# Performance work log

Measured on AMD Instinct MI355X. Metric: run time of the kernel, lower is better.

## Reference

```python
import jax, jax.numpy as jnp
import numpy as np

B, N, D = 8, 1024, 768
H = 12
HD = D // H


def setup_inputs() -> dict:
    key = jax.random.key(0)
    ks = jax.random.split(key, 9)
    s = 1.0 / np.sqrt(D)
    return {
        "x": jax.random.normal(ks[0], (B, N, D), dtype=jnp.float32),
        "Wq": jax.random.normal(ks[1], (D, D), dtype=jnp.float32) * s,
        "bq": jax.random.normal(ks[2], (D,), dtype=jnp.float32) * 0.02,
        "Wk": jax.random.normal(ks[3], (D, D), dtype=jnp.float32) * s,
        "bk": jax.random.normal(ks[4], (D,), dtype=jnp.float32) * 0.02,
        "Wv": jax.random.normal(ks[5], (D, D), dtype=jnp.float32) * s,
        "bv": jax.random.normal(ks[6], (D,), dtype=jnp.float32) * 0.02,
        "Wo": jax.random.normal(ks[7], (D, D), dtype=jnp.float32) * s,
        "bo": jax.random.normal(ks[8], (D,), dtype=jnp.float32) * 0.02,
    }


def _softmax_one(x):
    # quiet softmax: exp(x - max) / (1 + sum exp(x - max))
    x = x - jnp.max(x, axis=-1, keepdims=True)
    ex = jnp.exp(x)
    return ex / (1.0 + jnp.sum(ex, axis=-1, keepdims=True))


def reference(x, Wq, bq, Wk, bk, Wv, bv, Wo, bo):
    q = x @ Wq + bq  # [B,N,D]
    k = x @ Wk + bk
    v = x @ Wv + bv
    # split heads -> [B,H,N,HD]
    qs = q.reshape(B, N, H, HD).transpose(0, 2, 1, 3)
    ks = k.reshape(B, N, H, HD).transpose(0, 2, 1, 3)
    vs = v.reshape(B, N, H, HD).transpose(0, 2, 1, 3)
    scores = jnp.einsum("bhqd,bhkd->bhqk", qs, ks) / np.sqrt(HD)
    attn = _softmax_one(scores)  # quiet_attention=True
    ctx = jnp.einsum("bhqk,bhkd->bhqd", attn, vs)
    ctx = ctx.transpose(0, 2, 1, 3).reshape(B, N, D)
    return ctx @ Wo + bo
```

## Files before the change

kernel.cpp:

```cpp
#include <hip/hip_runtime.h>
#include <cstdint>

#define DEV __device__ __forceinline__

typedef __bf16 bf16x4 __attribute__((ext_vector_type(4)));
typedef __bf16 bf16x8 __attribute__((ext_vector_type(8)));
typedef float  floatx2 __attribute__((ext_vector_type(2)));
typedef float  floatx4 __attribute__((ext_vector_type(4)));
typedef float  floatx16 __attribute__((ext_vector_type(16)));
typedef unsigned uint4v __attribute__((ext_vector_type(4)));

constexpr int BB = 8, NSEQ = 1024, DMODEL = 768, NH = 12, HD = 64;
constexpr int MTOK = BB * NSEQ;
constexpr int NQKV = 3 * DMODEL;
constexpr float CS = 0.18033688011112042f;

DEV void async_copy16(void* lds, const void* g) {
    __builtin_amdgcn_global_load_lds(
        (__attribute__((address_space(1))) void*)(const_cast<void*>(g)),
        (__attribute__((address_space(3))) void*)lds,
        16, 0, 0);
}

DEV floatx4 mfma16x32(bf16x8 a, bf16x8 b, floatx4 c) {
    return __builtin_amdgcn_mfma_f32_16x16x32_bf16(a, b, c, 0, 0, 0);
}
DEV floatx16 mfma32x16(bf16x8 a, bf16x8 b, floatx16 c) {
    return __builtin_amdgcn_mfma_f32_32x32x16_bf16(a, b, c, 0, 0, 0);
}
DEV unsigned cvtpk(float a, float b) {
    unsigned r;
    asm("v_cvt_pk_bf16_f32 %0, %1, %2" : "=v"(r) : "v"(a), "v"(b));
    return r;
}
DEV void swap32(unsigned& x, unsigned& y) {
    asm("v_permlane32_swap_b32 %0, %1" : "+v"(x), "+v"(y));
}


__global__ __launch_bounds__(256) void k_prep(const float* __restrict__ x,
                                              __bf16* __restrict__ xb,
                                              const float* __restrict__ Wq,
                                              const float* __restrict__ Wk,
                                              const float* __restrict__ Wv,
                                              const float* __restrict__ Wo,
                                              __bf16* __restrict__ wtqkv,
                                              __bf16* __restrict__ wto,
                                              const float* __restrict__ bq,
                                              const float* __restrict__ bk,
                                              const float* __restrict__ bv,
                                              float* __restrict__ bqkv) {
    __shared__ float tile[32][33];
    int bid = blockIdx.x, t = threadIdx.x;
    if (bid < 6144) {
        int i = (bid * 256 + t) * 4;
        float4 v = *(const float4*)(x + i);
        bf16x4 o;
        o[0] = (__bf16)v.x; o[1] = (__bf16)v.y; o[2] = (__bf16)v.z; o[3] = (__bf16)v.w;
        *(bf16x4*)(xb + i) = o;
    } else if (bid < 8448) {
        int idx = bid - 6144;
        int z = idx / 576, rem = idx % 576;
        int k0 = (rem % 24) * 32, n0 = (rem / 24) * 32;
        const float* W = (z == 0) ? Wq : (z == 1) ? Wk : (z == 2) ? Wv : Wo;
        int tx = t & 31, ty = t >> 5;
#pragma unroll
        for (int p = 0; p < 4; p++)
            tile[ty + 8 * p][tx] = W[(size_t)(k0 + ty + 8 * p) * 768 + n0 + tx];
        __syncthreads();
        __bf16* out = (z < 3) ? (wtqkv + (size_t)z * 768 * 768) : wto;
#pragma unroll
        for (int p = 0; p < 4; p++)
            out[(size_t)(n0 + ty + 8 * p) * 768 + k0 + tx] = (__bf16)tile[tx][ty + 8 * p];
    } else {
        int i = (bid - 8448) * 256 + t;
        if (i < 768) bqkv[i] = bq[i];
        else if (i < 1536) bqkv[i] = bk[i - 768];
        else bqkv[i] = bv[i - 1536];
    }
}

__global__ __launch_bounds__(256) void k_qkv(const __bf16* __restrict__ A,
                                             const __bf16* __restrict__ Bt,
                                             const float* __restrict__ bias,
                                             __bf16* __restrict__ qfb,
                                             __bf16* __restrict__ kfb,
                                             __bf16* __restrict__ vfb) {
    constexpr int SLOT = 16384;
    __shared__ __align__(16) __bf16 lds[2 * SLOT];
    int t = threadIdx.x, lane = t & 63, w = t >> 6;
    int quad = lane >> 4, n16 = lane & 15;
    int wm = w & 1, wn = w >> 1;
    int m0 = blockIdx.x * 128, n0 = blockIdx.y * 128;
    floatx4 acc[4][4] = {};

    auto stage_tile = [&](__bf16* slot, int k0) {
        __bf16* As_ = slot;
        __bf16* Bs_ = slot + 8192;
#pragma unroll
        for (int i = 0; i < 4; i++) {
            int off = t + i * 256;
            int row = off >> 3, pc = off & 7;
            int c = pc ^ (row & 7);
            async_copy16(&As_[row * 64 + pc * 8],
                         &A[(size_t)(m0 + row) * 768 + k0 + c * 8]);
        }
#pragma unroll
        for (int i = 0; i < 4; i++) {
            int off = t + i * 256;
            int row = off >> 3, pc = off & 7;
            int c = pc ^ (row & 7);
            async_copy16(&Bs_[row * 64 + pc * 8],
                         &Bt[(size_t)(n0 + row) * 768 + k0 + c * 8]);
        }
    };

    stage_tile(lds, 0);

#pragma unroll
    for (int kt = 0; kt < 12; kt++) {
        __bf16* As_ = lds + (kt & 1) * SLOT;
        __bf16* Bs_ = As_ + 8192;

        if (kt + 1 < 12) stage_tile(lds + ((kt + 1) & 1) * SLOT, (kt + 1) * 64);
        __builtin_amdgcn_sched_barrier(0);
        if (kt + 1 < 12) {
            asm volatile("s_waitcnt vmcnt(8)\n\ts_barrier" ::: "memory");
        } else {
            asm volatile("s_waitcnt vmcnt(0)\n\ts_barrier" ::: "memory");
        }
        __builtin_amdgcn_sched_barrier(0);

#pragma unroll
        for (int kfi = 0; kfi < 2; kfi++) {
            bf16x8 a[4], bfr[4];
#pragma unroll
            for (int rt = 0; rt < 4; rt++) {
                int row = wm * 64 + rt * 16 + n16;
                a[rt] = *(const bf16x8*)&As_[row * 64 + ((quad + 4 * kfi) ^ (row & 7)) * 8];
            }
#pragma unroll
            for (int ct = 0; ct < 4; ct++) {
                int row = wn * 64 + ct * 16 + n16;
                bfr[ct] = *(const bf16x8*)&Bs_[row * 64 + ((quad + 4 * kfi) ^ (row & 7)) * 8];
            }
            __builtin_amdgcn_s_setprio(1);
#pragma unroll
            for (int rt = 0; rt < 4; rt++)
#pragma unroll
                for (int ct = 0; ct < 4; ct++)
                    acc[rt][ct] = mfma16x32(a[rt], bfr[ct], acc[rt][ct]);
            __builtin_amdgcn_s_setprio(0);
        }

        if (kt + 1 < 12) {
            __builtin_amdgcn_sched_barrier(0);
            asm volatile("s_barrier" ::: "memory");
            __builtin_amdgcn_sched_barrier(0);
        }
    }

    if (n0 >= 1536) {
#pragma unroll
        for (int ct = 0; ct < 4; ct++) {
            int col = n0 + wn * 64 + ct * 16 + n16;
            float bs = bias[col];
            int cz = col - 1536;
            int hh = cz >> 6, hd = cz & 63;
            int mg = hd >> 5, l5v = hd & 31;
#pragma unroll
            for (int rt = 0; rt < 4; rt++) {
                int row0 = m0 + wm * 64 + rt * 16 + quad * 4;
                int bb = row0 >> 10, key = row0 & 1023;
                int iw = key >> 7, w_ = (key >> 5) & 3, kc = (key >> 4) & 1;
                int b5v = (key >> 3) & 1, j0 = key & 7;
                bf16x4 pk;
#pragma unroll
                for (int r = 0; r < 4; r++) pk[r] = (__bf16)(acc[rt][ct][r] + bs);
                size_t idx = (((((size_t)(bb * 12 + hh) * 8 + iw) * 4 + w_) * 2 + kc) * 2 + mg) * 512
                             + (size_t)(b5v * 32 + l5v) * 8 + j0;
                *(bf16x4*)&vfb[idx] = pk;
            }
        }
    } else {
        __bf16* dst = (n0 < 768) ? qfb : kfb;
        float mult = (n0 < 768) ? CS : 1.0f;
        bool isQ = (n0 < 768);
        int cofs = isQ ? 0 : 768;
#pragma unroll
        for (int ct = 0; ct < 4; ct++) {
            int col = n0 + wn * 64 + ct * 16 + n16;
            float bs = bias[col];
            int cz = col - cofs;
            int hh = cz >> 6, hd = cz & 63;
            int kfi = hd >> 4, b5v = (hd >> 3) & 1, j = hd & 7;
#pragma unroll
            for (int rt = 0; rt < 4; rt++) {
                int row0 = m0 + wm * 64 + rt * 16 + quad * 4;
                int bb = row0 >> 10, q10 = row0 & 1023;
                size_t idx;
                if (isQ) {
                    int qt = q10 >> 5, l5v = q10 & 31;
                    idx = (((size_t)(bb * 12 + hh) * 32 + qt) * 4 + kfi) * 512
                          + (size_t)(b5v * 32 + l5v) * 8 + j;
                } else {
                    int iw = q10 >> 7, w_ = (q10 >> 5) & 3, l5v = q10 & 31;
                    idx = ((((size_t)(bb * 12 + hh) * 8 + iw) * 4 + w_) * 4 + kfi) * 512
                          + (size_t)(b5v * 32 + l5v) * 8 + j;
                }
#pragma unroll
                for (int r = 0; r < 4; r++)
                    dst[idx + (size_t)r * 8] = (__bf16)((acc[rt][ct][r] + bs) * mult);
            }
        }
    }
}

__global__ __launch_bounds__(256) void k_oproj(const __bf16* __restrict__ A,
                                               const __bf16* __restrict__ Bt,
                                               const float* __restrict__ bias,
                                               float* __restrict__ C) {
    constexpr int SLOT = 12288;
    __shared__ __align__(16) __bf16 lds[2 * SLOT];
    int t = threadIdx.x, lane = t & 63, w = t >> 6;
    int quad = lane >> 4, n16 = lane & 15;
    int wm = w & 1, wn = w >> 1;
    int m0 = blockIdx.x * 128, n0 = blockIdx.y * 64;
    floatx4 acc[4][2] = {};

    auto stage_tile = [&](__bf16* slot, int k0) {
        __bf16* As_ = slot;
        __bf16* Bs_ = slot + 8192;
#pragma unroll
        for (int i = 0; i < 4; i++) {
            int off = t + i * 256;
            int row = off >> 3, pc = off & 7;
            int c = pc ^ (row & 7);
            async_copy16(&As_[row * 64 + pc * 8],
                         &A[(size_t)(m0 + row) * 768 + k0 + c * 8]);
        }
#pragma unroll
        for (int i = 0; i < 2; i++) {
            int off = t + i * 256;
            int row = off >> 3, pc = off & 7;
            int c = pc ^ (row & 7);
            async_copy16(&Bs_[row * 64 + pc * 8],
                         &Bt[(size_t)(n0 + row) * 768 + k0 + c * 8]);
        }
    };

    stage_tile(lds, 0);

#pragma unroll
    for (int kt = 0; kt < 12; kt++) {
        __bf16* As_ = lds + (kt & 1) * SLOT;
        __bf16* Bs_ = As_ + 8192;

        if (kt + 1 < 12) stage_tile(lds + ((kt + 1) & 1) * SLOT, (kt + 1) * 64);
        __builtin_amdgcn_sched_barrier(0);
        if (kt + 1 < 12) {
            asm volatile("s_waitcnt vmcnt(6)\n\ts_barrier" ::: "memory");
        } else {
            asm volatile("s_waitcnt vmcnt(0)\n\ts_barrier" ::: "memory");
        }
        __builtin_amdgcn_sched_barrier(0);

#pragma unroll
        for (int kfi = 0; kfi < 2; kfi++) {
            bf16x8 a[4], bfr[2];
#pragma unroll
            for (int rt = 0; rt < 4; rt++) {
                int row = wm * 64 + rt * 16 + n16;
                a[rt] = *(const bf16x8*)&As_[row * 64 + ((quad + 4 * kfi) ^ (row & 7)) * 8];
            }
#pragma unroll
            for (int ct = 0; ct < 2; ct++) {
                int row = wn * 32 + ct * 16 + n16;
                bfr[ct] = *(const bf16x8*)&Bs_[row * 64 + ((quad + 4 * kfi) ^ (row & 7)) * 8];
            }
            __builtin_amdgcn_s_setprio(1);
#pragma unroll
            for (int rt = 0; rt < 4; rt++)
#pragma unroll
                for (int ct = 0; ct < 2; ct++)
                    acc[rt][ct] = mfma16x32(a[rt], bfr[ct], acc[rt][ct]);
            __builtin_amdgcn_s_setprio(0);
        }

        if (kt + 1 < 12) {
            __builtin_amdgcn_sched_barrier(0);
            asm volatile("s_barrier" ::: "memory");
            __builtin_amdgcn_sched_barrier(0);
        }
    }

#pragma unroll
    for (int ct = 0; ct < 2; ct++) {
        int col = n0 + wn * 32 + ct * 16 + n16;
        float bs = bias[col];
#pragma unroll
        for (int rt = 0; rt < 4; rt++) {
#pragma unroll
            for (int r = 0; r < 4; r++) {
                int row = m0 + wm * 64 + rt * 16 + quad * 4 + r;
                C[(size_t)row * DMODEL + col] = acc[rt][ct][r] + bs;
            }
        }
    }
}

__global__ __launch_bounds__(256) void k_attn(const __bf16* __restrict__ QF,
                                              const __bf16* __restrict__ KF,
                                              const __bf16* __restrict__ VF,
                                              __bf16* __restrict__ ctx) {
    int t = threadIdx.x, lane = t & 63, w = t >> 6;
    int l5 = lane & 31, b5 = lane >> 5;
    int id = blockIdx.x;
    int bB = id & 7;
    int seq = id >> 3;
    int h = seq % 12;
    int qb = seq / 12;
    int qt = qb * 4 + w;
    int bh = bB * NH + h;

    bf16x8 qf[4];
    {
        const __bf16* qp = QF + ((size_t)(bh * 32 + qt) * 4) * 512 + lane * 8;
#pragma unroll
        for (int kfi = 0; kfi < 4; kfi++)
            qf[kfi] = *(const bf16x8*)(qp + kfi * 512);
    }
    const __bf16* kp = KF + (size_t)(bh * 32) * 2048 + lane * 8;
    const __bf16* vp = VF + (size_t)(bh * 32) * 2048 + lane * 8;

    floatx16 acc[2] = {};
    floatx2 rs2 = {0.f, 0.f};
    float pm = 0.f;

    auto compute = [&](bf16x8 (&kf)[4], bf16x8 (&vf)[4]) {
        floatx16 s = {};
#pragma unroll
        for (int kfi = 0; kfi < 4; kfi++)
            s = mfma32x16(kf[kfi], qf[kfi], s);
        float p[16];
#pragma unroll
        for (int r = 0; r < 16; r++)
            p[r] = __builtin_amdgcn_exp2f(s[r]);
#pragma unroll
        for (int r = 0; r < 16; r += 2) {
            floatx2 pp = {p[r], p[r + 1]};
            rs2 += pp;
            pm = fmaxf(fmaxf(p[r], p[r + 1]), pm);
        }
        unsigned x0 = cvtpk(p[0], p[1]),   y0 = cvtpk(p[4], p[5]);
        unsigned x1 = cvtpk(p[2], p[3]),   y1 = cvtpk(p[6], p[7]);
        unsigned x2 = cvtpk(p[8], p[9]),   y2 = cvtpk(p[12], p[13]);
        unsigned x3 = cvtpk(p[10], p[11]), y3 = cvtpk(p[14], p[15]);
        swap32(x0, y0); swap32(x1, y1); swap32(x2, y2); swap32(x3, y3);
        uint4v pa = {x0, x1, y0, y1};
        uint4v pbv = {x2, x3, y2, y3};
        bf16x8 P0 = __builtin_bit_cast(bf16x8, pa);
        bf16x8 P1 = __builtin_bit_cast(bf16x8, pbv);
        acc[0] = mfma32x16(vf[0], P0, acc[0]);
        acc[1] = mfma32x16(vf[1], P0, acc[1]);
        acc[0] = mfma32x16(vf[2], P1, acc[0]);
        acc[1] = mfma32x16(vf[3], P1, acc[1]);
    };

    bf16x8 ka[4], kb[4], va[4], vb[4];
#pragma unroll
    for (int f = 0; f < 4; f++) ka[f] = *(const bf16x8*)(kp + f * 512);
#pragma unroll
    for (int f = 0; f < 4; f++) va[f] = *(const bf16x8*)(vp + f * 512);
    kp += 2048; vp += 2048;

    for (int c = 0; c < 32; c += 2) {
#pragma unroll
        for (int f = 0; f < 4; f++) kb[f] = *(const bf16x8*)(kp + f * 512);
#pragma unroll
        for (int f = 0; f < 4; f++) vb[f] = *(const bf16x8*)(vp + f * 512);
        kp += 2048; vp += 2048;
        compute(ka, va);
        if (c < 30) {
#pragma unroll
            for (int f = 0; f < 4; f++) ka[f] = *(const bf16x8*)(kp + f * 512);
#pragma unroll
            for (int f = 0; f < 4; f++) va[f] = *(const bf16x8*)(vp + f * 512);
            kp += 2048; vp += 2048;
        }
        compute(kb, vb);
    }

    float rs = rs2[0] + rs2[1];
    rs += __shfl_xor(rs, 32);
    pm = fmaxf(pm, __shfl_xor(pm, 32));
    float invd = 1.f / (pm + rs);

    __bf16* dst = ctx + ((size_t)(bB * NSEQ) + qt * 32 + l5) * DMODEL + h * 64;
#pragma unroll
    for (int mg = 0; mg < 2; mg++)
#pragma unroll
        for (int rq = 0; rq < 4; rq++) {
            bf16x4 o;
#pragma unroll
            for (int e = 0; e < 4; e++)
                o[e] = (__bf16)(acc[mg][rq * 4 + e] * invd);
            *(bf16x4*)(dst + mg * 32 + rq * 8 + b5 * 4) = o;
        }
}

extern "C" void kernel_launch(void* const* d_in, const int* in_sizes, int n_in,
                              void* d_out, int out_size, void* d_ws, size_t ws_size,
                              hipStream_t stream) {
    (void)in_sizes; (void)n_in; (void)out_size;
    const float* x  = (const float*)d_in[0];
    const float* Wq = (const float*)d_in[1];
    const float* bq = (const float*)d_in[2];
    const float* Wk = (const float*)d_in[3];
    const float* bk = (const float*)d_in[4];
    const float* Wv = (const float*)d_in[5];
    const float* bv = (const float*)d_in[6];
    const float* Wo = (const float*)d_in[7];
    const float* bo = (const float*)d_in[8];
    float* out = (float*)d_out;

    char* ws = (char*)d_ws;
    size_t off = 0;
    auto alloc = [&](size_t bytes) {
        void* p = ws + off;
        off += (bytes + 255) & ~(size_t)255;
        return p;
    };
    __bf16* xb    = (__bf16*)alloc((size_t)MTOK * DMODEL * 2);
    __bf16* wtqkv = (__bf16*)alloc((size_t)NQKV * DMODEL * 2);
    __bf16* wto   = (__bf16*)alloc((size_t)DMODEL * DMODEL * 2);
    float*  bqkv  = (float*)alloc((size_t)NQKV * 4);
    __bf16* qfb   = (__bf16*)alloc((size_t)MTOK * DMODEL * 2);
    __bf16* kfb   = (__bf16*)alloc((size_t)MTOK * DMODEL * 2);
    __bf16* vfb   = (__bf16*)alloc((size_t)MTOK * DMODEL * 2);
    if (off > ws_size) return;
    __bf16* ctx = xb;

    k_prep<<<dim3(8457), dim3(256), 0, stream>>>(x, xb, Wq, Wk, Wv, Wo, wtqkv, wto,
                                                 bq, bk, bv, bqkv);
    k_qkv<<<dim3(64, 18), dim3(256), 0, stream>>>(xb, wtqkv, bqkv, qfb, kfb, vfb);
    k_attn<<<dim3(768), dim3(256), 0, stream>>>(qfb, kfb, vfb, ctx);
    k_oproj<<<dim3(64, 12), dim3(256), 0, stream>>>(ctx, wto, bo, out);
}
```

Measured before the change: 177.5 us.

## Stage K/V tiles into LDS with async double-buffered global_load_lds in attention

```diff
diff --git a/kernel.cpp b/kernel.cpp
--- a/kernel.cpp
+++ b/kernel.cpp
@@ -313,6 +313,8 @@
                                               const __bf16* __restrict__ KF,
                                               const __bf16* __restrict__ VF,
                                               __bf16* __restrict__ ctx) {
+    constexpr int SLOT = 8192;
+    __shared__ __align__(16) __bf16 lds[2 * SLOT];
     int t = threadIdx.x, lane = t & 63, w = t >> 6;
     int l5 = lane & 31, b5 = lane >> 5;
     int id = blockIdx.x;
@@ -330,14 +332,36 @@
         for (int kfi = 0; kfi < 4; kfi++)
             qf[kfi] = *(const bf16x8*)(qp + kfi * 512);
     }
-    const __bf16* kp = KF + (size_t)(bh * 32) * 2048 + lane * 8;
-    const __bf16* vp = VF + (size_t)(bh * 32) * 2048 + lane * 8;
+    const __bf16* kbase = KF + (size_t)(bh * 32) * 2048;
+    const __bf16* vbase = VF + (size_t)(bh * 32) * 2048;
 
     floatx16 acc[2] = {};
     floatx2 rs2 = {0.f, 0.f};
     float pm = 0.f;
 
-    auto compute = [&](bf16x8 (&kf)[4], bf16x8 (&vf)[4]) {
+    auto stage = [&](int slot, int s) {
+        __bf16* ks = lds + slot * SLOT;
+        __bf16* vs = ks + 4096;
+#pragma unroll
+        for (int i = 0; i < 2; i++) {
+            int off = (t + i * 256) * 8;
+            async_copy16(&ks[off], &kbase[(size_t)s * 4096 + off]);
+        }
+#pragma unroll
+        for (int i = 0; i < 2; i++) {
+            int off = (t + i * 256) * 8;
+            async_copy16(&vs[off], &vbase[(size_t)s * 4096 + off]);
+        }
+    };
+
+    auto compute = [&](int slot, int cc) {
+        const __bf16* ks = lds + slot * SLOT + cc * 2048;
+        const __bf16* vs = lds + slot * SLOT + 4096 + cc * 2048;
+        bf16x8 kf[4], vf[4];
+#pragma unroll
+        for (int f = 0; f < 4; f++) kf[f] = *(const bf16x8*)&ks[f * 512 + lane * 8];
+#pragma unroll
+        for (int f = 0; f < 4; f++) vf[f] = *(const bf16x8*)&vs[f * 512 + lane * 8];
         floatx16 s = {};
 #pragma unroll
         for (int kfi = 0; kfi < 4; kfi++)
@@ -367,28 +391,25 @@
         acc[1] = mfma32x16(vf[3], P1, acc[1]);
     };
 
-    bf16x8 ka[4], kb[4], va[4], vb[4];
-#pragma unroll
-    for (int f = 0; f < 4; f++) ka[f] = *(const bf16x8*)(kp + f * 512);
-#pragma unroll
-    for (int f = 0; f < 4; f++) va[f] = *(const bf16x8*)(vp + f * 512);
-    kp += 2048; vp += 2048;
-
-    for (int c = 0; c < 32; c += 2) {
-#pragma unroll
-        for (int f = 0; f < 4; f++) kb[f] = *(const bf16x8*)(kp + f * 512);
-#pragma unroll
-        for (int f = 0; f < 4; f++) vb[f] = *(const bf16x8*)(vp + f * 512);
-        kp += 2048; vp += 2048;
-        compute(ka, va);
-        if (c < 30) {
-#pragma unroll
-            for (int f = 0; f < 4; f++) ka[f] = *(const bf16x8*)(kp + f * 512);
-#pragma unroll
-            for (int f = 0; f < 4; f++) va[f] = *(const bf16x8*)(vp + f * 512);
-            kp += 2048; vp += 2048;
-        }
-        compute(kb, vb);
+    stage(0, 0);
+
+    for (int s = 0; s < 16; s++) {
+        int cur = s & 1;
+        if (s + 1 < 16) stage(cur ^ 1, s + 1);
+        __builtin_amdgcn_sched_barrier(0);
+        if (s + 1 < 16) {
+            asm volatile("s_waitcnt vmcnt(4)\n\ts_barrier" ::: "memory");
+        } else {
+            asm volatile("s_waitcnt vmcnt(0)\n\ts_barrier" ::: "memory");
+        }
+        __builtin_amdgcn_sched_barrier(0);
+        compute(cur, 0);
+        compute(cur, 1);
+        if (s + 1 < 16) {
+            __builtin_amdgcn_sched_barrier(0);
+            asm volatile("s_barrier" ::: "memory");
+            __builtin_amdgcn_sched_barrier(0);
+        }
     }
 
     float rs = rs2[0] + rs2[1];
```

Result: slower. 182.0 us (+2.5%).

## Process two query tiles per wave in attention to reuse K/V fragments

Applied to the files above, without the earlier changes.

```diff
diff --git a/kernel.cpp b/kernel.cpp
--- a/kernel.cpp
+++ b/kernel.cpp
@@ -309,10 +309,10 @@
     }
 }
 
-__global__ __launch_bounds__(256) void k_attn(const __bf16* __restrict__ QF,
-                                              const __bf16* __restrict__ KF,
-                                              const __bf16* __restrict__ VF,
-                                              __bf16* __restrict__ ctx) {
+__global__ __launch_bounds__(128, 2) void k_attn(const __bf16* __restrict__ QF,
+                                                 const __bf16* __restrict__ KF,
+                                                 const __bf16* __restrict__ VF,
+                                                 __bf16* __restrict__ ctx) {
     int t = threadIdx.x, lane = t & 63, w = t >> 6;
     int l5 = lane & 31, b5 = lane >> 5;
     int id = blockIdx.x;
@@ -320,51 +320,84 @@
     int seq = id >> 3;
     int h = seq % 12;
     int qb = seq / 12;
-    int qt = qb * 4 + w;
+    int qt0 = qb * 4 + w * 2;
     int bh = bB * NH + h;
 
-    bf16x8 qf[4];
+    bf16x8 qf0[4], qf1[4];
     {
-        const __bf16* qp = QF + ((size_t)(bh * 32 + qt) * 4) * 512 + lane * 8;
-#pragma unroll
-        for (int kfi = 0; kfi < 4; kfi++)
-            qf[kfi] = *(const bf16x8*)(qp + kfi * 512);
+        const __bf16* qp = QF + ((size_t)(bh * 32 + qt0) * 4) * 512 + lane * 8;
+#pragma unroll
+        for (int kfi = 0; kfi < 4; kfi++) {
+            qf0[kfi] = *(const bf16x8*)(qp + kfi * 512);
+            qf1[kfi] = *(const bf16x8*)(qp + (4 + kfi) * 512);
+        }
     }
     const __bf16* kp = KF + (size_t)(bh * 32) * 2048 + lane * 8;
     const __bf16* vp = VF + (size_t)(bh * 32) * 2048 + lane * 8;
 
-    floatx16 acc[2] = {};
-    floatx2 rs2 = {0.f, 0.f};
-    float pm = 0.f;
+    floatx16 acc0[2] = {}, acc1[2] = {};
+    floatx2 rsa = {0.f, 0.f}, rsb = {0.f, 0.f};
+    float pma = 0.f, pmb = 0.f;
 
     auto compute = [&](bf16x8 (&kf)[4], bf16x8 (&vf)[4]) {
-        floatx16 s = {};
+        floatx16 s0 = {}, s1 = {};
 #pragma unroll
         for (int kfi = 0; kfi < 4; kfi++)
-            s = mfma32x16(kf[kfi], qf[kfi], s);
-        float p[16];
-#pragma unroll
-        for (int r = 0; r < 16; r++)
-            p[r] = __builtin_amdgcn_exp2f(s[r]);
-#pragma unroll
-        for (int r = 0; r < 16; r += 2) {
-            floatx2 pp = {p[r], p[r + 1]};
-            rs2 += pp;
-            pm = fmaxf(fmaxf(p[r], p[r + 1]), pm);
-        }
-        unsigned x0 = cvtpk(p[0], p[1]),   y0 = cvtpk(p[4], p[5]);
-        unsigned x1 = cvtpk(p[2], p[3]),   y1 = cvtpk(p[6], p[7]);
-        unsigned x2 = cvtpk(p[8], p[9]),   y2 = cvtpk(p[12], p[13]);
-        unsigned x3 = cvtpk(p[10], p[11]), y3 = cvtpk(p[14], p[15]);
-        swap32(x0, y0); swap32(x1, y1); swap32(x2, y2); swap32(x3, y3);
-        uint4v pa = {x0, x1, y0, y1};
-        uint4v pbv = {x2, x3, y2, y3};
-        bf16x8 P0 = __builtin_bit_cast(bf16x8, pa);
-        bf16x8 P1 = __builtin_bit_cast(bf16x8, pbv);
-        acc[0] = mfma32x16(vf[0], P0, acc[0]);
-        acc[1] = mfma32x16(vf[1], P0, acc[1]);
-        acc[0] = mfma32x16(vf[2], P1, acc[0]);
-        acc[1] = mfma32x16(vf[3], P1, acc[1]);
+            s0 = mfma32x16(kf[kfi], qf0[kfi], s0);
+#pragma unroll
+        for (int kfi = 0; kfi < 4; kfi++)
+            s1 = mfma32x16(kf[kfi], qf1[kfi], s1);
+
+        {
+            float p[16];
+#pragma unroll
+            for (int r = 0; r < 16; r++)
+                p[r] = __builtin_amdgcn_exp2f(s0[r]);
+#pragma unroll
+            for (int r = 0; r < 16; r += 2) {
+                floatx2 pp = {p[r], p[r + 1]};
+                rsa += pp;
+                pma = fmaxf(fmaxf(p[r], p[r + 1]), pma);
+            }
+            unsigned x0 = cvtpk(p[0], p[1]),   y0 = cvtpk(p[4], p[5]);
+            unsigned x1 = cvtpk(p[2], p[3]),   y1 = cvtpk(p[6], p[7]);
+            unsigned x2 = cvtpk(p[8], p[9]),   y2 = cvtpk(p[12], p[13]);
+            unsigned x3 = cvtpk(p[10], p[11]), y3 = cvtpk(p[14], p[15]);
+            swap32(x0, y0); swap32(x1, y1); swap32(x2, y2); swap32(x3, y3);
+            uint4v pa = {x0, x1, y0, y1};
+            uint4v pbv = {x2, x3, y2, y3};
+            bf16x8 P0 = __builtin_bit_cast(bf16x8, pa);
+            bf16x8 P1 = __builtin_bit_cast(bf16x8, pbv);
+            acc0[0] = mfma32x16(vf[0], P0, acc0[0]);
+            acc0[1] = mfma32x16(vf[1], P0, acc0[1]);
+            acc0[0] = mfma32x16(vf[2], P1, acc0[0]);
+            acc0[1] = mfma32x16(vf[3], P1, acc0[1]);
+        }
+        {
+            float p[16];
+#pragma unroll
+            for (int r = 0; r < 16; r++)
+                p[r] = __builtin_amdgcn_exp2f(s1[r]);
+#pragma unroll
+            for (int r = 0; r < 16; r += 2) {
+                floatx2 pp = {p[r], p[r + 1]};
+                rsb += pp;
+                pmb = fmaxf(fmaxf(p[r], p[r + 1]), pmb);
+            }
+            unsigned x0 = cvtpk(p[0], p[1]),   y0 = cvtpk(p[4], p[5]);
+            unsigned x1 = cvtpk(p[2], p[3]),   y1 = cvtpk(p[6], p[7]);
+            unsigned x2 = cvtpk(p[8], p[9]),   y2 = cvtpk(p[12], p[13]);
+            unsigned x3 = cvtpk(p[10], p[11]), y3 = cvtpk(p[14], p[15]);
+            swap32(x0, y0); swap32(x1, y1); swap32(x2, y2); swap32(x3, y3);
+            uint4v pa = {x0, x1, y0, y1};
+            uint4v pbv = {x2, x3, y2, y3};
+            bf16x8 P0 = __builtin_bit_cast(bf16x8, pa);
+            bf16x8 P1 = __builtin_bit_cast(bf16x8, pbv);
+            acc1[0] = mfma32x16(vf[0], P0, acc1[0]);
+            acc1[1] = mfma32x16(vf[1], P0, acc1[1]);
+            acc1[0] = mfma32x16(vf[2], P1, acc1[0]);
+            acc1[1] = mfma32x16(vf[3], P1, acc1[1]);
+        }
     };
 
     bf16x8 ka[4], kb[4], va[4], vb[4];
@@ -391,21 +424,29 @@
         compute(kb, vb);
     }
 
-    float rs = rs2[0] + rs2[1];
-    rs += __shfl_xor(rs, 32);
-    pm = fmaxf(pm, __shfl_xor(pm, 32));
-    float invd = 1.f / (pm + rs);
-
-    __bf16* dst = ctx + ((size_t)(bB * NSEQ) + qt * 32 + l5) * DMODEL + h * 64;
+    float rs0 = rsa[0] + rsa[1];
+    rs0 += __shfl_xor(rs0, 32);
+    pma = fmaxf(pma, __shfl_xor(pma, 32));
+    float invd0 = 1.f / (pma + rs0);
+    float rs1 = rsb[0] + rsb[1];
+    rs1 += __shfl_xor(rs1, 32);
+    pmb = fmaxf(pmb, __shfl_xor(pmb, 32));
+    float invd1 = 1.f / (pmb + rs1);
+
+    __bf16* dst0 = ctx + ((size_t)(bB * NSEQ) + qt0 * 32 + l5) * DMODEL + h * 64;
+    __bf16* dst1 = dst0 + (size_t)32 * DMODEL;
 #pragma unroll
     for (int mg = 0; mg < 2; mg++)
 #pragma unroll
         for (int rq = 0; rq < 4; rq++) {
-            bf16x4 o;
-#pragma unroll
-            for (int e = 0; e < 4; e++)
-                o[e] = (__bf16)(acc[mg][rq * 4 + e] * invd);
-            *(bf16x4*)(dst + mg * 32 + rq * 8 + b5 * 4) = o;
+            bf16x4 o0, o1;
+#pragma unroll
+            for (int e = 0; e < 4; e++) {
+                o0[e] = (__bf16)(acc0[mg][rq * 4 + e] * invd0);
+                o1[e] = (__bf16)(acc1[mg][rq * 4 + e] * invd1);
+            }
+            *(bf16x4*)(dst0 + mg * 32 + rq * 8 + b5 * 4) = o0;
+            *(bf16x4*)(dst1 + mg * 32 + rq * 8 + b5 * 4) = o1;
         }
 }
 
@@ -444,6 +485,6 @@
     k_prep<<<dim3(8457), dim3(256), 0, stream>>>(x, xb, Wq, Wk, Wv, Wo, wtqkv, wto,
                                                  bq, bk, bv, bqkv);
     k_qkv<<<dim3(64, 18), dim3(256), 0, stream>>>(xb, wtqkv, bqkv, qfb, kfb, vfb);
-    k_attn<<<dim3(768), dim3(256), 0, stream>>>(qfb, kfb, vfb, ctx);
+    k_attn<<<dim3(768), dim3(128), 0, stream>>>(qfb, kfb, vfb, ctx);
     k_oproj<<<dim3(64, 12), dim3(256), 0, stream>>>(ctx, wto, bo, out);
 }
```

Result: slower. 183.0 us (+3.1%).

## Shrink QKV GEMM N-tile to 64 and software-pipeline QK with softmax-PV in attention

Applied to the files above, without the earlier changes.

```diff
diff --git a/kernel.cpp b/kernel.cpp
--- a/kernel.cpp
+++ b/kernel.cpp
@@ -86,13 +86,13 @@
                                              __bf16* __restrict__ qfb,
                                              __bf16* __restrict__ kfb,
                                              __bf16* __restrict__ vfb) {
-    constexpr int SLOT = 16384;
+    constexpr int SLOT = 12288;
     __shared__ __align__(16) __bf16 lds[2 * SLOT];
     int t = threadIdx.x, lane = t & 63, w = t >> 6;
     int quad = lane >> 4, n16 = lane & 15;
     int wm = w & 1, wn = w >> 1;
-    int m0 = blockIdx.x * 128, n0 = blockIdx.y * 128;
-    floatx4 acc[4][4] = {};
+    int m0 = blockIdx.x * 128, n0 = blockIdx.y * 64;
+    floatx4 acc[4][2] = {};
 
     auto stage_tile = [&](__bf16* slot, int k0) {
         __bf16* As_ = slot;
@@ -106,7 +106,7 @@
                          &A[(size_t)(m0 + row) * 768 + k0 + c * 8]);
         }
 #pragma unroll
-        for (int i = 0; i < 4; i++) {
+        for (int i = 0; i < 2; i++) {
             int off = t + i * 256;
             int row = off >> 3, pc = off & 7;
             int c = pc ^ (row & 7);
@@ -125,7 +125,7 @@
         if (kt + 1 < 12) stage_tile(lds + ((kt + 1) & 1) * SLOT, (kt + 1) * 64);
         __builtin_amdgcn_sched_barrier(0);
         if (kt + 1 < 12) {
-            asm volatile("s_waitcnt vmcnt(8)\n\ts_barrier" ::: "memory");
+            asm volatile("s_waitcnt vmcnt(6)\n\ts_barrier" ::: "memory");
         } else {
             asm volatile("s_waitcnt vmcnt(0)\n\ts_barrier" ::: "memory");
         }
@@ -133,22 +133,22 @@
 
 #pragma unroll
         for (int kfi = 0; kfi < 2; kfi++) {
-            bf16x8 a[4], bfr[4];
+            bf16x8 a[4], bfr[2];
 #pragma unroll
             for (int rt = 0; rt < 4; rt++) {
                 int row = wm * 64 + rt * 16 + n16;
                 a[rt] = *(const bf16x8*)&As_[row * 64 + ((quad + 4 * kfi) ^ (row & 7)) * 8];
             }
 #pragma unroll
-            for (int ct = 0; ct < 4; ct++) {
-                int row = wn * 64 + ct * 16 + n16;
+            for (int ct = 0; ct < 2; ct++) {
+                int row = wn * 32 + ct * 16 + n16;
                 bfr[ct] = *(const bf16x8*)&Bs_[row * 64 + ((quad + 4 * kfi) ^ (row & 7)) * 8];
             }
             __builtin_amdgcn_s_setprio(1);
 #pragma unroll
             for (int rt = 0; rt < 4; rt++)
 #pragma unroll
-                for (int ct = 0; ct < 4; ct++)
+                for (int ct = 0; ct < 2; ct++)
                     acc[rt][ct] = mfma16x32(a[rt], bfr[ct], acc[rt][ct]);
             __builtin_amdgcn_s_setprio(0);
         }
@@ -162,8 +162,8 @@
 
     if (n0 >= 1536) {
 #pragma unroll
-        for (int ct = 0; ct < 4; ct++) {
-            int col = n0 + wn * 64 + ct * 16 + n16;
+        for (int ct = 0; ct < 2; ct++) {
+            int col = n0 + wn * 32 + ct * 16 + n16;
             float bs = bias[col];
             int cz = col - 1536;
             int hh = cz >> 6, hd = cz & 63;
@@ -188,8 +188,8 @@
         bool isQ = (n0 < 768);
         int cofs = isQ ? 0 : 768;
 #pragma unroll
-        for (int ct = 0; ct < 4; ct++) {
-            int col = n0 + wn * 64 + ct * 16 + n16;
+        for (int ct = 0; ct < 2; ct++) {
+            int col = n0 + wn * 32 + ct * 16 + n16;
             float bs = bias[col];
             int cz = col - cofs;
             int hh = cz >> 6, hd = cz & 63;
@@ -337,11 +337,14 @@
     floatx2 rs2 = {0.f, 0.f};
     float pm = 0.f;
 
-    auto compute = [&](bf16x8 (&kf)[4], bf16x8 (&vf)[4]) {
+    auto qk = [&](bf16x8 (&kf)[4]) {
         floatx16 s = {};
 #pragma unroll
         for (int kfi = 0; kfi < 4; kfi++)
             s = mfma32x16(kf[kfi], qf[kfi], s);
+        return s;
+    };
+    auto fin = [&](floatx16 s, bf16x8 (&vf)[4]) {
         float p[16];
 #pragma unroll
         for (int r = 0; r < 16; r++)
@@ -367,28 +370,38 @@
         acc[1] = mfma32x16(vf[3], P1, acc[1]);
     };
 
-    bf16x8 ka[4], kb[4], va[4], vb[4];
-#pragma unroll
-    for (int f = 0; f < 4; f++) ka[f] = *(const bf16x8*)(kp + f * 512);
-#pragma unroll
-    for (int f = 0; f < 4; f++) va[f] = *(const bf16x8*)(vp + f * 512);
+    bf16x8 k0[4], v0[4], k1[4], v1[4];
+#pragma unroll
+    for (int f = 0; f < 4; f++) k0[f] = *(const bf16x8*)(kp + f * 512);
+#pragma unroll
+    for (int f = 0; f < 4; f++) v0[f] = *(const bf16x8*)(vp + f * 512);
     kp += 2048; vp += 2048;
-
-    for (int c = 0; c < 32; c += 2) {
-#pragma unroll
-        for (int f = 0; f < 4; f++) kb[f] = *(const bf16x8*)(kp + f * 512);
-#pragma unroll
-        for (int f = 0; f < 4; f++) vb[f] = *(const bf16x8*)(vp + f * 512);
+    floatx16 s0 = qk(k0);
+
+    for (int c = 1; c < 31; c += 2) {
+#pragma unroll
+        for (int f = 0; f < 4; f++) k1[f] = *(const bf16x8*)(kp + f * 512);
+#pragma unroll
+        for (int f = 0; f < 4; f++) v1[f] = *(const bf16x8*)(vp + f * 512);
         kp += 2048; vp += 2048;
-        compute(ka, va);
-        if (c < 30) {
-#pragma unroll
-            for (int f = 0; f < 4; f++) ka[f] = *(const bf16x8*)(kp + f * 512);
-#pragma unroll
-            for (int f = 0; f < 4; f++) va[f] = *(const bf16x8*)(vp + f * 512);
-            kp += 2048; vp += 2048;
-        }
-        compute(kb, vb);
+        floatx16 s1 = qk(k1);
+        fin(s0, v0);
+#pragma unroll
+        for (int f = 0; f < 4; f++) k0[f] = *(const bf16x8*)(kp + f * 512);
+#pragma unroll
+        for (int f = 0; f < 4; f++) v0[f] = *(const bf16x8*)(vp + f * 512);
+        kp += 2048; vp += 2048;
+        s0 = qk(k0);
+        fin(s1, v1);
+    }
+    {
+#pragma unroll
+        for (int f = 0; f < 4; f++) k1[f] = *(const bf16x8*)(kp + f * 512);
+#pragma unroll
+        for (int f = 0; f < 4; f++) v1[f] = *(const bf16x8*)(vp + f * 512);
+        floatx16 s1 = qk(k1);
+        fin(s0, v0);
+        fin(s1, v1);
     }
 
     float rs = rs2[0] + rs2[1];
@@ -443,7 +456,7 @@
 
     k_prep<<<dim3(8457), dim3(256), 0, stream>>>(x, xb, Wq, Wk, Wv, Wo, wtqkv, wto,
                                                  bq, bk, bv, bqkv);
-    k_qkv<<<dim3(64, 18), dim3(256), 0, stream>>>(xb, wtqkv, bqkv, qfb, kfb, vfb);
+    k_qkv<<<dim3(64, 36), dim3(256), 0, stream>>>(xb, wtqkv, bqkv, qfb, kfb, vfb);
     k_attn<<<dim3(768), dim3(256), 0, stream>>>(qfb, kfb, vfb, ctx);
     k_oproj<<<dim3(64, 12), dim3(256), 0, stream>>>(ctx, wto, bo, out);
 }
```

Result: no change. 176.0 us (-0.9%).
